# Kernel optimization log

Hardware: AMD Instinct MI355X
Metric: run time of the kernel (lower is better)

Reference implementation:

```python
import jax, jax.numpy as jnp
import numpy as np


def setup_inputs() -> dict:
    key = jax.random.key(0)
    ks = jax.random.split(key, 11)
    B, N, C, E, O = 16, 2048, 64, 16, 64
    H, M, K = 16, 2, 2  # hyperGNN_dim, middle_dim, cheb_k
    s = 0.1
    return {
        "x": jax.random.normal(ks[0], (B, N, C), dtype=jnp.float32),
        "emb0": jax.random.normal(ks[1], (B, N, E), dtype=jnp.float32),
        "emb1": jax.random.normal(ks[2], (N, E), dtype=jnp.float32),
        "w1": jax.random.normal(ks[3], (C, H), dtype=jnp.float32) * s,
        "b1": jnp.zeros((H,), dtype=jnp.float32),
        "w2": jax.random.normal(ks[4], (H, M), dtype=jnp.float32) * s,
        "b2": jnp.zeros((M,), dtype=jnp.float32),
        "w3": jax.random.normal(ks[5], (M, E), dtype=jnp.float32) * s,
        "b3": jnp.zeros((E,), dtype=jnp.float32),
        "weights_pool": jax.random.normal(ks[6], (E, K, C, O), dtype=jnp.float32) * s,
        "bias_pool": jax.random.normal(ks[7], (E, O), dtype=jnp.float32) * s,
    }


def reference(x, emb0, emb1, w1, b1, w2, b2, w3, b3, weights_pool, bias_pool):
    # hypernetwork MLP: Linear -> sigmoid -> Linear -> sigmoid -> Linear
    h = jax.nn.sigmoid(x @ w1 + b1)
    h = jax.nn.sigmoid(h @ w2 + b2)
    filt = h @ w3 + b3                                   # (B,N,E)
    nodevec = jnp.tanh(emb0 * filt)                      # (B,N,E)
    # dynamic adjacency: relu(nodevec @ nodevec^T)
    adj = jax.nn.relu(jnp.einsum('bnd,bmd->bnm', nodevec, nodevec))  # (B,N,N)
    # normalized Laplacian: D^{-1/2} A D^{-1/2} (diag_embed expressed via broadcast)
    d = jnp.sum(adj, axis=-1) ** (-0.5)                  # (B,N)
    L = d[:, :, None] * adj * d[:, None, :]              # (B,N,N)
    # supports1 is identity -> x_g1 == x
    x_g1 = x
    x_g2 = jnp.einsum('bnm,bmc->bnc', L, x)
    x_g = jnp.stack([x_g1, x_g2], axis=2)                # (B,N,K=2,C)
    # per-node hypernetwork weights and bias
    weights = jnp.einsum('nd,dkio->nkio', emb1, weights_pool)  # (N,K,C,O)
    bias = emb1 @ bias_pool                               # (N,O)
    out = jnp.einsum('bnki,nkio->bno', x_g, weights) + bias
    return out
```

## Files before the change

### kernel.cpp

```cpp
#include <hip/hip_runtime.h>
#include <hip/hip_bf16.h>

#define B_ 16
#define N_ 2048
#define C_ 64
#define E_ 16
#define O_ 64
#define H_ 16

typedef __attribute__((ext_vector_type(8)))  short short8;
typedef __attribute__((ext_vector_type(16))) float f32x16;

#define NVB_OFF   0u
#define RSP_OFF   262144u
#define XST_OFF   393216u
#define YT_OFF    1441792u
#define XGALL_OFF 9830400u
#define WPB_OFF   11927552u
#define E1B_OFF   11993600u

__device__ __forceinline__ unsigned short f2bf(float f) {
  union { float f; unsigned int u; } v; v.f = f;
  unsigned int r = v.u + 0x7FFFu + ((v.u >> 16) & 1u);
  return (unsigned short)(r >> 16);
}

#define CVT_PK(dst, lo_, hi_) \
  asm("v_cvt_pk_bf16_f32 %0, %1, %2" : "=v"(dst) : "v"(lo_), "v"(hi_))
#define PL_SWAP(x_, y_) \
  asm("v_permlane32_swap_b32 %0, %1" : "+v"(x_), "+v"(y_))

__global__ __launch_bounds__(256) void k0_prep(
    const float* __restrict__ wp, const float* __restrict__ bp,
    const float* __restrict__ emb1,
    unsigned short* __restrict__ wpB, unsigned short* __restrict__ emb1b)
{
  int id = blockIdx.x * 256 + threadIdx.x;
  if (id < 132096) {
    int t = id & 7, o = (id >> 3) & 63, rest = id >> 9;
    int sub = rest & 1, kc = rest >> 1;
    int q2 = sub * 8 + t;
    float v = (kc < 128) ? wp[(size_t)(kc * 16 + q2) * 64 + o]
                         : bp[(size_t)q2 * 64 + o];
    wpB[id] = f2bf(v);
  } else {
    int id2 = id - 132096;
    emb1b[id2] = f2bf(emb1[id2]);
  }
}

__global__ __launch_bounds__(256) void k1_hyper(
    const float* __restrict__ x, const float* __restrict__ emb0,
    const float* __restrict__ w1, const float* __restrict__ b1,
    const float* __restrict__ w2, const float* __restrict__ b2,
    const float* __restrict__ w3, const float* __restrict__ b3,
    unsigned short* __restrict__ nvb, unsigned short* __restrict__ xgall)
{
  __shared__ float w1s[C_*H_];
  __shared__ float b1s[H_], w2s[H_*2], b2s[2], w3s[2*E_], b3s[E_];
  int tid = threadIdx.x;
  for (int i = tid; i < C_*H_; i += 256) w1s[i] = w1[i];
  if (tid < H_)   b1s[tid] = b1[tid];
  if (tid < H_*2) w2s[tid] = w2[tid];
  if (tid < 2)    b2s[tid] = b2[tid];
  if (tid < 2*E_) w3s[tid] = w3[tid];
  if (tid < E_)   b3s[tid] = b3[tid];
  __syncthreads();

  int idx = blockIdx.x * 256 + tid;
  float xr[C_];
  const float4* xp = reinterpret_cast<const float4*>(x + (size_t)idx * C_);
  #pragma unroll
  for (int j = 0; j < 16; ++j) {
    float4 v = xp[j];
    xr[4*j] = v.x; xr[4*j+1] = v.y; xr[4*j+2] = v.z; xr[4*j+3] = v.w;
  }
  unsigned short xus[C_];
  #pragma unroll
  for (int c = 0; c < C_; ++c) xus[c] = f2bf(xr[c]);
  unsigned short* xo = xgall + (size_t)idx * 128;
  #pragma unroll
  for (int j = 0; j < 8; ++j)
    reinterpret_cast<uint4*>(xo)[j] = reinterpret_cast<uint4*>(xus)[j];

  float h1[H_];
  #pragma unroll
  for (int h = 0; h < H_; ++h) h1[h] = b1s[h];
  #pragma unroll 8
  for (int c = 0; c < C_; ++c) {
    float xv = xr[c];
    #pragma unroll
    for (int j = 0; j < 4; ++j) {
      float4 w = reinterpret_cast<const float4*>(&w1s[c*H_])[j];
      h1[4*j]   = fmaf(xv, w.x, h1[4*j]);
      h1[4*j+1] = fmaf(xv, w.y, h1[4*j+1]);
      h1[4*j+2] = fmaf(xv, w.z, h1[4*j+2]);
      h1[4*j+3] = fmaf(xv, w.w, h1[4*j+3]);
    }
  }
  #pragma unroll
  for (int h = 0; h < H_; ++h) h1[h] = 1.f / (1.f + __expf(-h1[h]));
  float a0 = b2s[0], a1 = b2s[1];
  #pragma unroll
  for (int h = 0; h < H_; ++h) {
    a0 = fmaf(h1[h], w2s[h*2],   a0);
    a1 = fmaf(h1[h], w2s[h*2+1], a1);
  }
  a0 = 1.f / (1.f + __expf(-a0));
  a1 = 1.f / (1.f + __expf(-a1));

  const float4* ep = reinterpret_cast<const float4*>(emb0 + (size_t)idx * E_);
  unsigned short us[E_];
  #pragma unroll
  for (int j = 0; j < 4; ++j) {
    float4 e = ep[j];
    int c = 4*j;
    us[c]   = f2bf(tanhf(e.x * (b3s[c]   + a0*w3s[c]   + a1*w3s[E_+c])));
    us[c+1] = f2bf(tanhf(e.y * (b3s[c+1] + a0*w3s[c+1] + a1*w3s[E_+c+1])));
    us[c+2] = f2bf(tanhf(e.z * (b3s[c+2] + a0*w3s[c+2] + a1*w3s[E_+c+2])));
    us[c+3] = f2bf(tanhf(e.w * (b3s[c+3] + a0*w3s[c+3] + a1*w3s[E_+c+3])));
  }
  *reinterpret_cast<short8*>(nvb + (size_t)idx * E_)     = *reinterpret_cast<short8*>(&us[0]);
  *reinterpret_cast<short8*>(nvb + (size_t)idx * E_ + 8) = *reinterpret_cast<short8*>(&us[8]);
}

__global__ __launch_bounds__(256, 4) void p1_rowsum(
    const unsigned short* __restrict__ nvb, float* __restrict__ rsp)
{
  int tid = threadIdx.x, lane = tid & 63, wid = tid >> 6;
  int lo = lane & 31, hi = lane >> 5;
  int orig = blockIdx.x;
  int eff = (orig & 7) * 128 + (orig >> 3);
  int rb = eff & 15, b = (eff >> 4) & 15, part = eff >> 8;
  int N0 = rb * 128 + wid * 32;

  short8 bfrag = *reinterpret_cast<const short8*>(
      nvb + ((size_t)b * N_ + N0 + lo) * E_ + 8 * hi);
  f32x16 zero = {};
  float rs = 0.f;
  const unsigned short* abase =
      nvb + ((size_t)b * N_ + part * 512 + lo) * E_ + 8 * hi;
  #pragma unroll 2
  for (int mc = 0; mc < 16; ++mc) {
    short8 afrag = *reinterpret_cast<const short8*>(abase + (size_t)mc * 32 * E_);
    f32x16 p = __builtin_amdgcn_mfma_f32_32x32x16_bf16(afrag, bfrag, zero, 0, 0, 0);
    #pragma unroll
    for (int r = 0; r < 16; ++r) rs += fmaxf(p[r], 0.f);
  }
  rs += __shfl_xor(rs, 32, 64);
  if (lane < 32) rsp[((size_t)part * B_ + b) * N_ + N0 + lo] = rs;
}

__global__ __launch_bounds__(256) void p2_scaleT(
    const float* __restrict__ x, const float* __restrict__ rsp,
    unsigned short* __restrict__ xsT)
{
  int tid = threadIdx.x;
  int c = tid & 63, g = tid >> 6;
  int m0 = blockIdx.x * 128 + g * 32;
  int b  = blockIdx.y;
  const float* rp = rsp + (size_t)b * N_;
  const size_t RST = (size_t)B_ * N_;
  unsigned int pk[16];
  #pragma unroll
  for (int k = 0; k < 32; ++k) {
    int m = m0 + k;
    float s = rp[m] + rp[RST + m] + rp[2*RST + m] + rp[3*RST + m];
    float d = rsqrtf(s);
    float v = d * x[((size_t)b * N_ + m) * C_ + c];
    unsigned short us = f2bf(v);
    if (k & 1) pk[k >> 1] |= ((unsigned int)us) << 16;
    else       pk[k >> 1]  = us;
  }
  unsigned short* o = xsT + (((size_t)b * 64 + (m0 >> 5)) * 64 + c) * 32;
  #pragma unroll
  for (int j = 0; j < 4; ++j)
    reinterpret_cast<uint4*>(o)[j] = *reinterpret_cast<uint4*>(&pk[4*j]);
}

__global__ __launch_bounds__(256, 4) void p3_spmm(
    const unsigned short* __restrict__ nvb, const unsigned short* __restrict__ xsT,
    float* __restrict__ yT)
{
  int tid = threadIdx.x, lane = tid & 63, wid = tid >> 6;
  int lo = lane & 31, hi = lane >> 5;
  int orig = blockIdx.x;
  int eff = (orig & 7) * 128 + (orig >> 3);
  int rb = eff & 15, b = (eff >> 4) & 15, part = eff >> 8;
  int N0 = rb * 128 + wid * 32;

  short8 bfrag = *reinterpret_cast<const short8*>(
      nvb + ((size_t)b * N_ + N0 + lo) * E_ + 8 * hi);
  f32x16 acc0 = {}, acc1 = {};
  f32x16 zero = {};
  const unsigned short* abase =
      nvb + ((size_t)b * N_ + part * 512 + lo) * E_ + 8 * hi;
  const unsigned short* xtile =
      xsT + (((size_t)b * 64 + part * 16) * 64) * 32 + lo * 32 + 8 * hi;

  #pragma unroll 2
  for (int mc = 0; mc < 16; ++mc) {
    short8 afrag = *reinterpret_cast<const short8*>(abase + (size_t)mc * 32 * E_);
    const unsigned short* xt = xtile + (size_t)mc * 2048;
    short8 x00 = *reinterpret_cast<const short8*>(xt);
    short8 x01 = *reinterpret_cast<const short8*>(xt + 16);
    short8 x10 = *reinterpret_cast<const short8*>(xt + 1024);
    short8 x11 = *reinterpret_cast<const short8*>(xt + 1024 + 16);

    f32x16 p = __builtin_amdgcn_mfma_f32_32x32x16_bf16(afrag, bfrag, zero, 0, 0, 0);
    float q[16];
    #pragma unroll
    for (int r = 0; r < 16; ++r) q[r] = fmaxf(p[r], 0.f);

    unsigned int A0, Bb0, C0, D0, A1, Bb1, C1, D1;
    CVT_PK(A0,  q[0],  q[1]);  CVT_PK(Bb0, q[2],  q[3]);
    CVT_PK(C0,  q[4],  q[5]);  CVT_PK(D0,  q[6],  q[7]);
    CVT_PK(A1,  q[8],  q[9]);  CVT_PK(Bb1, q[10], q[11]);
    CVT_PK(C1,  q[12], q[13]); CVT_PK(D1,  q[14], q[15]);
    PL_SWAP(A0, C0);  PL_SWAP(Bb0, D0);
    PL_SWAP(A1, C1);  PL_SWAP(Bb1, D1);

    union { unsigned int u[4]; short8 s; } f0, f1;
    f0.u[0] = A0; f0.u[1] = Bb0; f0.u[2] = C0; f0.u[3] = D0;
    f1.u[0] = A1; f1.u[1] = Bb1; f1.u[2] = C1; f1.u[3] = D1;

    acc0 = __builtin_amdgcn_mfma_f32_32x32x16_bf16(x00, f0.s, acc0, 0, 0, 0);
    acc0 = __builtin_amdgcn_mfma_f32_32x32x16_bf16(x01, f1.s, acc0, 0, 0, 0);
    acc1 = __builtin_amdgcn_mfma_f32_32x32x16_bf16(x10, f0.s, acc1, 0, 0, 0);
    acc1 = __builtin_amdgcn_mfma_f32_32x32x16_bf16(x11, f1.s, acc1, 0, 0, 0);
  }

  float* yb = yT + ((size_t)part * B_ + b) * C_ * N_;
  #pragma unroll
  for (int r = 0; r < 16; ++r) {
    int cl = (r & 3) + 8 * (r >> 2) + 4 * hi;
    yb[(size_t)cl * N_ + N0 + lo]        = acc0[r];
    yb[(size_t)(cl + 32) * N_ + N0 + lo] = acc1[r];
  }
}

__global__ __launch_bounds__(256) void p4_xg2(
    const float* __restrict__ yT, const float* __restrict__ rsp,
    unsigned short* __restrict__ xgall)
{
  __shared__ unsigned short tile[64][72];
  int tid = threadIdx.x;
  int nl = tid & 63, cg = tid >> 6;
  int n0 = blockIdx.x * 64, b = blockIdx.y;
  int n = n0 + nl;
  const size_t RST = (size_t)B_ * N_;
  float rs = rsp[(size_t)b * N_ + n]       + rsp[RST + (size_t)b * N_ + n]
           + rsp[2*RST + (size_t)b * N_ + n] + rsp[3*RST + (size_t)b * N_ + n];
  float dn = rsqrtf(rs);
  const float* y0 = yT + (size_t)b * C_ * N_;
  const size_t PST = (size_t)B_ * C_ * N_;
  #pragma unroll
  for (int cc = 0; cc < 16; cc += 2) {
    int c = cg * 16 + cc;
    size_t o0 = (size_t)c * N_ + n, o1 = (size_t)(c+1) * N_ + n;
    float v0 = y0[o0] + y0[PST + o0] + y0[2*PST + o0] + y0[3*PST + o0];
    float v1 = y0[o1] + y0[PST + o1] + y0[2*PST + o1] + y0[3*PST + o1];
    unsigned int pk = (unsigned int)f2bf(dn * v0) | ((unsigned int)f2bf(dn * v1) << 16);
    *reinterpret_cast<unsigned int*>(&tile[nl][c]) = pk;
  }
  __syncthreads();
  int q = tid & 3, j = tid >> 2;
  uint4 va = *reinterpret_cast<const uint4*>(&tile[j][q*16]);
  uint4 vb = *reinterpret_cast<const uint4*>(&tile[j][q*16 + 8]);
  unsigned short* o = xgall + ((size_t)b * N_ + n0 + j) * 128 + 64 + q * 16;
  *reinterpret_cast<uint4*>(o)     = va;
  *reinterpret_cast<uint4*>(o + 8) = vb;
}

__global__ __launch_bounds__(256) void k5_out(
    const unsigned short* __restrict__ xgall, const unsigned short* __restrict__ emb1b,
    const float* __restrict__ emb1, const unsigned short* __restrict__ wpB,
    float* __restrict__ out)
{
  int tid = threadIdx.x, lane = tid & 63, wid = tid >> 6;
  int lo = lane & 31, hi = lane >> 5;
  int gw = blockIdx.x * 4 + wid;
  int mt = gw >> 1;
  int o0 = (gw & 1) * 32;
  int M0 = mt * 32;
  int n0 = M0 & (N_ - 1);

  const unsigned short* arow = xgall + (size_t)(M0 + lo) * 128 + 8 * hi;
  short8 a[8];
  #pragma unroll
  for (int c8 = 0; c8 < 8; ++c8)
    a[c8] = *reinterpret_cast<const short8*>(arow + c8 * 16);
  short8 abias = *reinterpret_cast<const short8*>(
      emb1b + (size_t)(n0 + lo) * E_ + 8 * hi);

  f32x16 acc = {};
  f32x16 kzero = {};

  int nr[16];
  #pragma unroll
  for (int r = 0; r < 16; ++r) nr[r] = n0 + (r & 3) + 8 * (r >> 2) + 4 * hi;

  #pragma unroll 2
  for (int dg = 0; dg < 8; ++dg) {
    float2 e2[16];
    #pragma unroll
    for (int r = 0; r < 16; ++r)
      e2[r] = *reinterpret_cast<const float2*>(emb1 + (size_t)nr[r] * E_ + dg * 2);
    #pragma unroll
    for (int dd = 0; dd < 2; ++dd) {
      int d = dg * 2 + dd;
      const unsigned short* bbase = wpB + ((size_t)((d * 8) * 2 + hi) * 64 + o0 + lo) * 8;
      f32x16 t0 = kzero, t1 = kzero;
      #pragma unroll
      for (int c8 = 0; c8 < 8; c8 += 2) {
        short8 B0 = *reinterpret_cast<const short8*>(bbase + (size_t)(c8    ) * 1024);
        short8 B1 = *reinterpret_cast<const short8*>(bbase + (size_t)(c8 + 1) * 1024);
        t0 = __builtin_amdgcn_mfma_f32_32x32x16_bf16(a[c8],     B0, t0, 0, 0, 0);
        t1 = __builtin_amdgcn_mfma_f32_32x32x16_bf16(a[c8 + 1], B1, t1, 0, 0, 0);
      }
      #pragma unroll
      for (int r = 0; r < 16; ++r) {
        float e = dd ? e2[r].y : e2[r].x;
        acc[r] = fmaf(e, t0[r] + t1[r], acc[r]);
      }
    }
  }
  {
    const unsigned short* bbase = wpB + ((size_t)(256 + hi) * 64 + o0 + lo) * 8;
    short8 Bb = *reinterpret_cast<const short8*>(bbase);
    acc = __builtin_amdgcn_mfma_f32_32x32x16_bf16(abias, Bb, acc, 0, 0, 0);
  }
  #pragma unroll
  for (int r = 0; r < 16; ++r) {
    int cl = (r & 3) + 8 * (r >> 2) + 4 * hi;
    out[(size_t)(M0 + cl) * O_ + o0 + lo] = acc[r];
  }
}

extern "C" void kernel_launch(void* const* d_in, const int* in_sizes, int n_in,
                              void* d_out, int out_size, void* d_ws, size_t ws_size,
                              hipStream_t stream)
{
  const float* x    = (const float*)d_in[0];
  const float* emb0 = (const float*)d_in[1];
  const float* emb1 = (const float*)d_in[2];
  const float* w1   = (const float*)d_in[3];
  const float* b1   = (const float*)d_in[4];
  const float* w2   = (const float*)d_in[5];
  const float* b2   = (const float*)d_in[6];
  const float* w3   = (const float*)d_in[7];
  const float* b3   = (const float*)d_in[8];
  const float* wp   = (const float*)d_in[9];
  const float* bp   = (const float*)d_in[10];
  float* out = (float*)d_out;
  float* ws  = (float*)d_ws;

  unsigned short* nvb   = (unsigned short*)(ws + NVB_OFF);
  float*          rsp   = ws + RSP_OFF;
  unsigned short* xsT   = (unsigned short*)(ws + XST_OFF);
  float*          yT    = ws + YT_OFF;
  unsigned short* xgall = (unsigned short*)(ws + XGALL_OFF);
  unsigned short* wpB   = (unsigned short*)(ws + WPB_OFF);
  unsigned short* emb1b = (unsigned short*)(ws + E1B_OFF);

  k0_prep  <<<644, 256, 0, stream>>>(wp, bp, emb1, wpB, emb1b);
  k1_hyper <<<128, 256, 0, stream>>>(x, emb0, w1, b1, w2, b2, w3, b3, nvb, xgall);
  p1_rowsum<<<1024, 256, 0, stream>>>(nvb, rsp);
  p2_scaleT<<<dim3(16,16), 256, 0, stream>>>(x, rsp, xsT);
  p3_spmm  <<<1024, 256, 0, stream>>>(nvb, xsT, yT);
  p4_xg2   <<<dim3(32,16), 256, 0, stream>>>(yT, rsp, xgall);
  k5_out   <<<512, 256, 0, stream>>>(xgall, emb1b, emb1, wpB, out);
}
```

Measured before the change: 178.5 us.

## Fuse prep into hypernet kernel, stage x via LDS, store SpMM partials as bf16

```diff
diff --git a/kernel.cpp b/kernel.cpp
--- a/kernel.cpp
+++ b/kernel.cpp
@@ -15,66 +15,85 @@
 #define RSP_OFF   262144u
 #define XST_OFF   393216u
 #define YT_OFF    1441792u
-#define XGALL_OFF 9830400u
-#define WPB_OFF   11927552u
-#define E1B_OFF   11993600u
+#define XGALL_OFF 5636096u
+#define WPB_OFF   7733248u
+#define E1B_OFF   7799296u
 
 __device__ __forceinline__ unsigned short f2bf(float f) {
   union { float f; unsigned int u; } v; v.f = f;
   unsigned int r = v.u + 0x7FFFu + ((v.u >> 16) & 1u);
   return (unsigned short)(r >> 16);
 }
+__device__ __forceinline__ float bf2f(unsigned short u) {
+  union { unsigned int i; float f; } v; v.i = ((unsigned int)u) << 16;
+  return v.f;
+}
 
 #define CVT_PK(dst, lo_, hi_) \
   asm("v_cvt_pk_bf16_f32 %0, %1, %2" : "=v"(dst) : "v"(lo_), "v"(hi_))
 #define PL_SWAP(x_, y_) \
   asm("v_permlane32_swap_b32 %0, %1" : "+v"(x_), "+v"(y_))
 
-__global__ __launch_bounds__(256) void k0_prep(
-    const float* __restrict__ wp, const float* __restrict__ bp,
-    const float* __restrict__ emb1,
-    unsigned short* __restrict__ wpB, unsigned short* __restrict__ emb1b)
-{
-  int id = blockIdx.x * 256 + threadIdx.x;
-  if (id < 132096) {
-    int t = id & 7, o = (id >> 3) & 63, rest = id >> 9;
-    int sub = rest & 1, kc = rest >> 1;
-    int q2 = sub * 8 + t;
-    float v = (kc < 128) ? wp[(size_t)(kc * 16 + q2) * 64 + o]
-                         : bp[(size_t)q2 * 64 + o];
-    wpB[id] = f2bf(v);
-  } else {
-    int id2 = id - 132096;
-    emb1b[id2] = f2bf(emb1[id2]);
-  }
-}
-
-__global__ __launch_bounds__(256) void k1_hyper(
+__global__ __launch_bounds__(256) void k01_fused(
     const float* __restrict__ x, const float* __restrict__ emb0,
     const float* __restrict__ w1, const float* __restrict__ b1,
     const float* __restrict__ w2, const float* __restrict__ b2,
     const float* __restrict__ w3, const float* __restrict__ b3,
-    unsigned short* __restrict__ nvb, unsigned short* __restrict__ xgall)
-{
+    const float* __restrict__ wp, const float* __restrict__ bp,
+    const float* __restrict__ emb1,
+    unsigned short* __restrict__ nvb, unsigned short* __restrict__ xgall,
+    unsigned short* __restrict__ wpB, unsigned short* __restrict__ emb1b)
+{
+  int tid = threadIdx.x;
+  if (blockIdx.x >= 128) {
+    int id = (blockIdx.x - 128) * 256 + tid;
+    if (id < 132096) {
+      int t = id & 7, o = (id >> 3) & 63, rest = id >> 9;
+      int sub = rest & 1, kc = rest >> 1;
+      int q2 = sub * 8 + t;
+      float v = (kc < 128) ? wp[(size_t)(kc * 16 + q2) * 64 + o]
+                           : bp[(size_t)q2 * 64 + o];
+      wpB[id] = f2bf(v);
+    } else {
+      int id2 = id - 132096;
+      emb1b[id2] = f2bf(emb1[id2]);
+    }
+    return;
+  }
+
+  __shared__ float xt[128][65];
   __shared__ float w1s[C_*H_];
   __shared__ float b1s[H_], w2s[H_*2], b2s[2], w3s[2*E_], b3s[E_];
-  int tid = threadIdx.x;
   for (int i = tid; i < C_*H_; i += 256) w1s[i] = w1[i];
   if (tid < H_)   b1s[tid] = b1[tid];
   if (tid < H_*2) w2s[tid] = w2[tid];
   if (tid < 2)    b2s[tid] = b2[tid];
   if (tid < 2*E_) w3s[tid] = w3[tid];
   if (tid < E_)   b3s[tid] = b3[tid];
-  __syncthreads();
-
-  int idx = blockIdx.x * 256 + tid;
+
+  int base = blockIdx.x * 256;
   float xr[C_];
-  const float4* xp = reinterpret_cast<const float4*>(x + (size_t)idx * C_);
-  #pragma unroll
-  for (int j = 0; j < 16; ++j) {
-    float4 v = xp[j];
-    xr[4*j] = v.x; xr[4*j+1] = v.y; xr[4*j+2] = v.z; xr[4*j+3] = v.w;
-  }
+  #pragma unroll
+  for (int ph = 0; ph < 2; ++ph) {
+    const float4* src = reinterpret_cast<const float4*>(x + (size_t)(base + ph*128) * C_);
+    #pragma unroll
+    for (int j = 0; j < 8; ++j) {
+      int i = j * 256 + tid;
+      float4 v = src[i];
+      int row = i >> 4, c4 = (i & 15) * 4;
+      xt[row][c4]   = v.x; xt[row][c4+1] = v.y;
+      xt[row][c4+2] = v.z; xt[row][c4+3] = v.w;
+    }
+    __syncthreads();
+    if ((tid >> 7) == ph) {
+      int lr = tid & 127;
+      #pragma unroll
+      for (int j = 0; j < C_; ++j) xr[j] = xt[lr][j];
+    }
+    __syncthreads();
+  }
+
+  int idx = base + tid;
   unsigned short xus[C_];
   #pragma unroll
   for (int c = 0; c < C_; ++c) xus[c] = f2bf(xr[c]);
@@ -180,7 +199,7 @@
 
 __global__ __launch_bounds__(256, 4) void p3_spmm(
     const unsigned short* __restrict__ nvb, const unsigned short* __restrict__ xsT,
-    float* __restrict__ yT)
+    unsigned short* __restrict__ yT)
 {
   int tid = threadIdx.x, lane = tid & 63, wid = tid >> 6;
   int lo = lane & 31, hi = lane >> 5;
@@ -230,17 +249,17 @@
     acc1 = __builtin_amdgcn_mfma_f32_32x32x16_bf16(x11, f1.s, acc1, 0, 0, 0);
   }
 
-  float* yb = yT + ((size_t)part * B_ + b) * C_ * N_;
+  unsigned short* yb = yT + ((size_t)part * B_ + b) * C_ * N_;
   #pragma unroll
   for (int r = 0; r < 16; ++r) {
     int cl = (r & 3) + 8 * (r >> 2) + 4 * hi;
-    yb[(size_t)cl * N_ + N0 + lo]        = acc0[r];
-    yb[(size_t)(cl + 32) * N_ + N0 + lo] = acc1[r];
+    yb[(size_t)cl * N_ + N0 + lo]        = f2bf(acc0[r]);
+    yb[(size_t)(cl + 32) * N_ + N0 + lo] = f2bf(acc1[r]);
   }
 }
 
 __global__ __launch_bounds__(256) void p4_xg2(
-    const float* __restrict__ yT, const float* __restrict__ rsp,
+    const unsigned short* __restrict__ yT, const float* __restrict__ rsp,
     unsigned short* __restrict__ xgall)
 {
   __shared__ unsigned short tile[64][72];
@@ -249,17 +268,17 @@
   int n0 = blockIdx.x * 64, b = blockIdx.y;
   int n = n0 + nl;
   const size_t RST = (size_t)B_ * N_;
-  float rs = rsp[(size_t)b * N_ + n]       + rsp[RST + (size_t)b * N_ + n]
+  float rs = rsp[(size_t)b * N_ + n]         + rsp[RST + (size_t)b * N_ + n]
            + rsp[2*RST + (size_t)b * N_ + n] + rsp[3*RST + (size_t)b * N_ + n];
   float dn = rsqrtf(rs);
-  const float* y0 = yT + (size_t)b * C_ * N_;
+  const unsigned short* y0 = yT + (size_t)b * C_ * N_;
   const size_t PST = (size_t)B_ * C_ * N_;
   #pragma unroll
   for (int cc = 0; cc < 16; cc += 2) {
     int c = cg * 16 + cc;
     size_t o0 = (size_t)c * N_ + n, o1 = (size_t)(c+1) * N_ + n;
-    float v0 = y0[o0] + y0[PST + o0] + y0[2*PST + o0] + y0[3*PST + o0];
-    float v1 = y0[o1] + y0[PST + o1] + y0[2*PST + o1] + y0[3*PST + o1];
+    float v0 = bf2f(y0[o0]) + bf2f(y0[PST + o0]) + bf2f(y0[2*PST + o0]) + bf2f(y0[3*PST + o0]);
+    float v1 = bf2f(y0[o1]) + bf2f(y0[PST + o1]) + bf2f(y0[2*PST + o1]) + bf2f(y0[3*PST + o1]);
     unsigned int pk = (unsigned int)f2bf(dn * v0) | ((unsigned int)f2bf(dn * v1) << 16);
     *reinterpret_cast<unsigned int*>(&tile[nl][c]) = pk;
   }
@@ -358,13 +377,13 @@
   unsigned short* nvb   = (unsigned short*)(ws + NVB_OFF);
   float*          rsp   = ws + RSP_OFF;
   unsigned short* xsT   = (unsigned short*)(ws + XST_OFF);
-  float*          yT    = ws + YT_OFF;
+  unsigned short* yT    = (unsigned short*)(ws + YT_OFF);
   unsigned short* xgall = (unsigned short*)(ws + XGALL_OFF);
   unsigned short* wpB   = (unsigned short*)(ws + WPB_OFF);
   unsigned short* emb1b = (unsigned short*)(ws + E1B_OFF);
 
-  k0_prep  <<<644, 256, 0, stream>>>(wp, bp, emb1, wpB, emb1b);
-  k1_hyper <<<128, 256, 0, stream>>>(x, emb0, w1, b1, w2, b2, w3, b3, nvb, xgall);
+  k01_fused<<<772, 256, 0, stream>>>(x, emb0, w1, b1, w2, b2, w3, b3,
+                                     wp, bp, emb1, nvb, xgall, wpB, emb1b);
   p1_rowsum<<<1024, 256, 0, stream>>>(nvb, rsp);
   p2_scaleT<<<dim3(16,16), 256, 0, stream>>>(x, rsp, xsT);
   p3_spmm  <<<1024, 256, 0, stream>>>(nvb, xsT, yT);
```

After: 177.4 us. About the same (-0.6%).
